# Kernel tuning notes

Hardware: AMD Instinct MI355X
Metric: run time of the kernel (lower is better)

## Reference

```python
import jax, jax.numpy as jnp
import numpy as np

N_REACHES = 4096
N_STEPS = 96
DT = 3600.0  # routing timestep (s), default from MuskingumCungeRouter


def safe_pow(base, exp, eps=1e-6):
    # AD-safe power: exp(e * log(max(b, eps)))
    return jnp.exp(exp * jnp.log(jnp.maximum(base, eps)))


def setup_inputs() -> dict:
    key = jax.random.key(0)
    ks = jax.random.split(key, 10)
    n, T = N_REACHES, N_STEPS
    u = lambda k, lo, hi, shape: jax.random.uniform(k, shape, minval=lo, maxval=hi)
    lateral_inflows = u(ks[0], 0.0, 5.0, (T, n))          # m^3/s lateral inflow
    initial_Q = u(ks[1], 0.1, 10.0, (n,))
    lengths = u(ks[2], 500.0, 10000.0, (n,))              # reach length (m)
    slopes = u(ks[3], 1e-4, 0.05, (n,))                   # bed slope
    manning_n = u(ks[4], 0.02, 0.08, (n,))
    width_coef = u(ks[5], 2.0, 10.0, (n,))
    width_exp = u(ks[6], 0.4, 0.6, (n,))                  # ~0.5 typical
    depth_coef = u(ks[7], 0.2, 0.6, (n,))
    depth_exp = u(ks[8], 0.25, 0.35, (n,))                # ~0.3 typical
    # Strictly lower-triangular sparse adjacency: reach i receives from j < i
    # (valid topological order), ~4 upstream links per reach on average.
    upstream_mask = jnp.tril(jax.random.uniform(ks[9], (n, n)) < (4.0 / n), k=-1)
    is_outlet = jnp.arange(n) == n - 1
    return dict(lateral_inflows=lateral_inflows, initial_Q=initial_Q,
                lengths=lengths, slopes=slopes, manning_n=manning_n,
                width_coef=width_coef, width_exp=width_exp,
                depth_coef=depth_coef, depth_exp=depth_exp,
                upstream_mask=upstream_mask, is_outlet=is_outlet)


def _mc_coeffs(Q, L, S, mn, wc, we, dc, de, dt):
    """Vectorized Muskingum-Cunge coefficients for all reaches.

    Faithful fusion of compute_channel_geometry -> compute_velocity_manning ->
    compute_celerity -> compute_muskingum_params. Q here is Q_ref = max(state.Q, 0.1),
    which only depends on the previous state, so hoisting out of the per-reach
    scan is mathematically identical to the original.
    """
    Qs = jnp.maximum(Q, 0.01)
    W = wc * safe_pow(Qs, we)
    D = dc * safe_pow(Qs, de)
    A = W * D
    R = A / (W + 2.0 * D)                      # hydraulic radius
    safe_S = jnp.maximum(S, 1e-6)
    V = (1.0 / jnp.maximum(mn, 1e-3)) * safe_pow(R, 2.0 / 3.0) * jnp.sqrt(safe_S)
    c = jnp.maximum((5.0 / 3.0) * V, 0.01)     # kinematic wave celerity
    K = jnp.maximum(L / c, dt * 0.1)
    X = jnp.clip(0.5 * (1.0 - Q / (W * c * safe_S * L + 1e-6)), 0.0, 0.5)
    den = 2.0 * K * (1.0 - X) + dt
    C0 = jnp.maximum((dt - 2.0 * K * X) / den, 0.0)
    C1 = jnp.maximum((dt + 2.0 * K * X) / den, 0.0)
    C2 = jnp.maximum((2.0 * K * (1.0 - X) - dt) / den, 0.0)
    tot = C0 + C1 + C2
    return C0 / tot, C1 / tot, C2 / tot


def _route(lateral_inflows, initial_Q, lengths, slopes, manning_n,
           width_coef, width_exp, depth_coef, depth_exp,
           upstream_mask, is_outlet, dt=DT):
    n = lengths.shape[0]

    def step(state, lateral):
        Q, Q_prev, I_prev = state
        Q_ref = jnp.maximum(Q, 0.1)
        C0, C1, C2 = _mc_coeffs(Q_ref, lengths, slopes, manning_n,
                                width_coef, width_exp, depth_coef, depth_exp, dt)

        # Sequential topological sweep: masked reduction over already-routed reaches.
        def process(Q_acc, i):
            upstream_Q = jnp.sum(jnp.where(upstream_mask[i], Q_acc, 0.0))
            I_curr = upstream_Q + lateral[i]
            Q_out = jnp.maximum(C0[i] * I_curr + C1[i] * I_prev[i] + C2[i] * Q_prev[i], 0.0)
            return Q_acc.at[i].set(Q_out), I_curr

        Q_final, I_all = jax.lax.scan(process, jnp.zeros(n, lateral.dtype), jnp.arange(n))
        outlet_Q = jnp.sum(jnp.where(is_outlet, Q_final, 0.0))
        return (Q_final, Q, I_all), outlet_Q

    init = (initial_Q, initial_Q, jnp.zeros(n, initial_Q.dtype))
    _, outlet_series = jax.lax.scan(step, init, lateral_inflows)
    return outlet_series  # [n_timesteps]


def reference(lateral_inflows, initial_Q, lengths, slopes, manning_n,
              width_coef, width_exp, depth_coef, depth_exp,
              upstream_mask, is_outlet):
    return _route(lateral_inflows, initial_Q, lengths, slopes, manning_n,
                  width_coef, width_exp, depth_coef, depth_exp,
                  upstream_mask, is_outlet)
```

## Files before the change

### kernel.cpp

```cpp
#include <hip/hip_runtime.h>

#define NR 4096
#define NT 96
#define NNZ_CAP 10240
#define SREM_CAP 4096
#define LONG_CAP 4096
#define WLDS 8
#define SSTR 4112
#define SHORTLAG 7
#define DHIST 32
#define DTSTEP 3600.0f
#define LOG2_1E6 -19.931568f

__device__ __forceinline__ float RCP(float x) { return __builtin_amdgcn_rcpf(x); }
__device__ __forceinline__ float EXP2(float x) { return __builtin_amdgcn_exp2f(x); }
__device__ __forceinline__ float LOG2(float x) { return __builtin_amdgcn_logf(x); }

__device__ __forceinline__ void phase_barrier() {
  asm volatile("s_waitcnt lgkmcnt(0) vmcnt(6)" ::: "memory");
  __builtin_amdgcn_s_barrier();
  asm volatile("" ::: "memory");
}

__global__ void mc_build(const int* __restrict__ mask, int* __restrict__ rowBase,
                         int* __restrict__ rowCnt, int* __restrict__ gctr,
                         unsigned short* __restrict__ cols) {
  __shared__ unsigned short tmp[80];
  __shared__ int baseS;
  int row = blockIdx.x;
  int lane = threadIdx.x;
  const int* rs = mask + (size_t)row * NR;
  int total = 0;
  for (int j0 = 0; j0 < NR; j0 += 64) {
    int j = j0 + lane;
    int pred = (rs[j] != 0);
    unsigned long long m = __ballot(pred);
    if (pred) {
      int pos = total + __popcll(m & ((1ull << lane) - 1ull));
      if (pos < 80) tmp[pos] = (unsigned short)j;
    }
    total += __popcll(m);
  }
  if (total > 80) total = 80;
  if (lane == 0) {
    int b = atomicAdd(gctr, total);
    rowBase[row] = b;
    rowCnt[row] = total;
    baseS = b;
  }
  __syncthreads();
  int base = baseS;
  for (int e = lane; e < total; e += 64) {
    int p = base + e;
    if (p < NNZ_CAP) cols[p] = tmp[e];
  }
}

__global__ __launch_bounds__(1024) void mc_prep(
    const int* __restrict__ rowBase, const int* __restrict__ rowCnt,
    const int* __restrict__ gctr, const unsigned short* __restrict__ colsOld,
    unsigned short* __restrict__ orderG, unsigned short* __restrict__ levNG,
    unsigned short* __restrict__ scolG, unsigned int* __restrict__ sremMeta,
    unsigned int* __restrict__ longMeta, unsigned short* __restrict__ sremG,
    unsigned short* __restrict__ longG, unsigned char* __restrict__ lsG,
    int* __restrict__ meta) {
  __shared__ unsigned short cols_s[NNZ_CAP];
  __shared__ unsigned char lev_s[NR];
  __shared__ unsigned short newid_s[NR];
  __shared__ unsigned short order_s[NR];
  __shared__ unsigned char lsrc_s[NR];
  __shared__ int cnt[1024];
  __shared__ int sbuf[1024];
  __shared__ int flagA[40];
  __shared__ int maxLevS;
  const int tid = threadIdx.x;
  int nnz = gctr[0];
  if (nnz > NNZ_CAP) nnz = NNZ_CAP;
  for (int e = tid; e < nnz; e += 1024) cols_s[e] = colsOld[e];
  for (int i = tid; i < 40; i += 1024) flagA[i] = 0;

  int b_r[4], e_r[4];
#pragma unroll
  for (int k = 0; k < 4; ++k) {
    int i = 4 * tid + k;
    int b = rowBase[i];
    if (b > NNZ_CAP) b = NNZ_CAP;
    int e = b + rowCnt[i];
    if (e > NNZ_CAP) e = NNZ_CAP;
    b_r[k] = b;
    e_r[k] = e;
    lev_s[i] = 0;
    lsrc_s[i] = 0;
  }
  if (tid == 0) maxLevS = 0;
  __syncthreads();

  for (int pass = 0; pass < 34; ++pass) {
    int ch = 0;
#pragma unroll
    for (int k = 0; k < 4; ++k) {
      int i = 4 * tid + k;
      int lv = 0;
      for (int e = b_r[k]; e < e_r[k]; ++e) {
        int l2 = (int)lev_s[cols_s[e]] + 1;
        lv = lv > l2 ? lv : l2;
      }
      if (lv > 60) lv = 60;
      if (lv > (int)lev_s[i]) {
        lev_s[i] = (unsigned char)lv;
        ch = 1;
      }
    }
    if (ch) flagA[pass] = 1;
    __syncthreads();
    if (flagA[pass] == 0) break;
  }
  int lm = 0;
#pragma unroll
  for (int k = 0; k < 4; ++k) {
    int l = lev_s[4 * tid + k];
    lm = lm > l ? lm : l;
  }
  atomicMax(&maxLevS, lm);
  __syncthreads();
  const int maxLev = maxLevS;
  if (tid == 0) {
    meta[0] = maxLev + 1;
    meta[2] = (maxLev >= 32) ? 1 : 0;
  }
  if (maxLev >= 32) {
#pragma unroll
    for (int k = 0; k < 4; ++k) {
      int i = 4 * tid + k;
      orderG[i] = (unsigned short)i;
      levNG[i] = (unsigned short)lev_s[i];
    }
    return;
  }

  cnt[tid] = 0;
  __syncthreads();
  int bkt_r[4];
#pragma unroll
  for (int k = 0; k < 4; ++k) {
    int i = 4 * tid + k;
    int d = e_r[k] - b_r[k];
    if (d > 31) d = 31;
    int bkt = ((int)lev_s[i]) * 32 + d;
    bkt_r[k] = bkt;
    atomicAdd(&cnt[bkt], 1);
  }
  __syncthreads();
  int v = cnt[tid];
  sbuf[tid] = v;
  __syncthreads();
  for (int off = 1; off < 1024; off <<= 1) {
    int add = tid >= off ? sbuf[tid - off] : 0;
    __syncthreads();
    sbuf[tid] += add;
    __syncthreads();
  }
  cnt[tid] = sbuf[tid] - v;
  __syncthreads();
#pragma unroll
  for (int k = 0; k < 4; ++k) {
    int i = 4 * tid + k;
    int pos = atomicAdd(&cnt[bkt_r[k]], 1);
    order_s[pos] = (unsigned short)i;
    newid_s[i] = (unsigned short)pos;
  }
  __syncthreads();

#pragma unroll
  for (int k = 0; k < 4; ++k) {
    int p = 4 * tid + k;
    int oldi = order_s[p];
    orderG[p] = (unsigned short)oldi;
    int lp = (int)lev_s[oldi];
    levNG[p] = (unsigned short)lp;
    int b = rowBase[oldi];
    if (b > NNZ_CAP) b = NNZ_CAP;
    int e = b + rowCnt[oldi];
    if (e > NNZ_CAP) e = NNZ_CAP;
    int nS = 0, nR = 0, nL = 0;
    for (int ee = b; ee < e; ++ee) {
      int lag = lp - (int)lev_s[cols_s[ee]];
      if (lag <= SHORTLAG) {
        if (nS < 4) ++nS; else ++nR;
      } else ++nL;
    }
    if (nR > 63) nR = 63;
    if (nL > 63) nL = 63;
    int sB = nR ? atomicAdd(&meta[4], nR) : 0;
    int lB = nL ? atomicAdd(&meta[5], nL) : 0;
    if (sB > SREM_CAP) sB = SREM_CAP;
    if (sB + nR > SREM_CAP) nR = SREM_CAP - sB;
    if (lB > LONG_CAP) lB = LONG_CAP;
    if (lB + nL > LONG_CAP) nL = LONG_CAP - lB;
    unsigned short sc[4] = {4096, 4096, 4096, 4096};
    int iS = 0, cR = 0, cL = 0;
    for (int ee = b; ee < e; ++ee) {
      int cOld = cols_s[ee];
      int cN = newid_s[cOld];
      int lag = lp - (int)lev_s[cOld];
      if (lag <= SHORTLAG) {
        if (iS < 4) sc[iS++] = (unsigned short)cN;
        else if (cR < nR) { sremG[sB + cR] = (unsigned short)cN; ++cR; }
      } else {
        if (cL < nL) { longG[lB + cL] = (unsigned short)cN; ++cL; }
        lsrc_s[cN] = 1;
      }
    }
    scolG[4 * p + 0] = sc[0];
    scolG[4 * p + 1] = sc[1];
    scolG[4 * p + 2] = sc[2];
    scolG[4 * p + 3] = sc[3];
    sremMeta[p] = (unsigned)sB | ((unsigned)nR << 20) | ((unsigned)iS << 26);
    longMeta[p] = (unsigned)lB | ((unsigned)nL << 20);
  }
  if (tid == 0) meta[1] = newid_s[NR - 1];
  __syncthreads();
#pragma unroll
  for (int k = 0; k < 4; ++k) {
    int p = 4 * tid + k;
    lsG[p] = lsrc_s[p];
  }
}

__global__ void mc_permlat(const float* __restrict__ lat,
                           const unsigned short* __restrict__ orderG,
                           float* __restrict__ latP) {
  int g = blockIdx.x * 256 + threadIdx.x;
  int t = g >> 12, p = g & 4095;
  latP[g] = lat[t * NR + orderG[p]];
}

__global__ __launch_bounds__(1024, 4) void mc_route(
    const float* __restrict__ lat, const float* __restrict__ latP,
    const float* __restrict__ initQ, const float* __restrict__ Lg,
    const float* __restrict__ Sg, const float* __restrict__ mng,
    const float* __restrict__ wcg, const float* __restrict__ weg,
    const float* __restrict__ dcg, const float* __restrict__ deg,
    const int* __restrict__ rowBase, const int* __restrict__ rowCnt,
    const unsigned short* __restrict__ colsOld,
    const unsigned short* __restrict__ orderG,
    const unsigned short* __restrict__ levNG,
    const unsigned short* __restrict__ scolG,
    const unsigned int* __restrict__ sremMeta,
    const unsigned int* __restrict__ longMeta,
    const unsigned short* __restrict__ sremG,
    const unsigned short* __restrict__ longG,
    const unsigned char* __restrict__ lsG, const int* __restrict__ meta,
    float* Qhist, float* __restrict__ out, int usePerm) {
  __shared__ float win_s[WLDS * SSTR];
  __shared__ unsigned short srem_s[SREM_CAP];
  __shared__ unsigned short long_s[LONG_CAP];
  const int tid = threadIdx.x;
  const int nlv = meta[0];
  const int fb = meta[2];
  const int outletNew = meta[1];
  const float* latB = usePerm ? latP : lat;

  if (!fb) {
    int sc_r[4][4];
    int lev_r[4], io_r[4], ls_r[4], wOff_r[4], nsc_r[4];
    unsigned int smeta_r[4], lmeta_r[4];
    const float* latcol_r[4];
    float lwc_r[4], we_r[4], ldc_r[4], de_r[4], lvk_r[4], lgSL_r[4], L_r[4];
    float ip_r[4], q1_r[4], q2_r[4], latN_r[4];
    float latv_r[4], sup_r[4], C0_r[4], C1_r[4], C2_r[4];

    int nSrem = meta[4];
    if (nSrem > SREM_CAP) nSrem = SREM_CAP;
    int nLong = meta[5];
    if (nLong > LONG_CAP) nLong = LONG_CAP;
    for (int e = tid; e < nSrem; e += 1024) srem_s[e] = sremG[e];
    for (int e = tid; e < nLong; e += 1024) long_s[e] = longG[e];
    if (tid < WLDS) win_s[tid * SSTR + 4096] = 0.f;

#pragma unroll
    for (int k = 0; k < 4; ++k) {
      int p = tid + k * 1024;
      int oldi = orderG[p];
      lev_r[k] = (int)levNG[p];
      uint2 cc = *(const uint2*)(scolG + 4 * p);
      sc_r[k][0] = cc.x & 0xFFFFu;
      sc_r[k][1] = cc.x >> 16;
      sc_r[k][2] = cc.y & 0xFFFFu;
      sc_r[k][3] = cc.y >> 16;
      smeta_r[k] = sremMeta[p];
      nsc_r[k] = (int)(smeta_r[k] >> 26);
      lmeta_r[k] = longMeta[p];
      ls_r[k] = (int)lsG[p];
      io_r[k] = (p == outletNew);
      float Lv = Lg[oldi];
      float sS = fmaxf(Sg[oldi], 1e-6f);
      float mnv = fmaxf(mng[oldi], 1e-3f);
      lvk_r[k] = 0.7369656f + 0.5f * LOG2(sS) - LOG2(mnv);
      lgSL_r[k] = LOG2(sS * Lv);
      L_r[k] = Lv;
      lwc_r[k] = LOG2(wcg[oldi]);
      we_r[k] = weg[oldi];
      ldc_r[k] = LOG2(dcg[oldi]);
      de_r[k] = deg[oldi];
      float q0 = initQ[oldi];
      q1_r[k] = q0;
      q2_r[k] = q0;
      ip_r[k] = 0.f;
      wOff_r[k] = 0;
      latcol_r[k] = latB + (usePerm ? p : oldi);
      latN_r[k] = *latcol_r[k];
    }
    __syncthreads();

#define BG(k, tt)                                                               \
  {                                                                             \
    latv_r[k] = latN_r[k];                                                      \
    int tn = (tt) + 1;                                                          \
    tn = tn < NT ? tn : NT - 1;                                                 \
    latN_r[k] = latcol_r[k][tn << 12];                                          \
    const int wB = wOff_r[k];                                                   \
    float v0 = win_s[wB + sc_r[k][0]];                                          \
    float v1 = win_s[wB + sc_r[k][1]];                                          \
    float v23 = 0.f;                                                            \
    if (nsc_r[k] > 2)                                                           \
      v23 = win_s[wB + sc_r[k][2]] + win_s[wB + sc_r[k][3]];                    \
    float ssum = 0.f;                                                           \
    const int sC = (int)((smeta_r[k] >> 20) & 63);                              \
    if (sC) {                                                                   \
      const int sB = (int)(smeta_r[k] & 0xFFFFFu);                              \
      for (int e = 0; e < sC; ++e) ssum += win_s[wB + srem_s[sB + e]];          \
    }                                                                           \
    float lsum = 0.f;                                                           \
    const int lC = (int)(lmeta_r[k] >> 20);                                     \
    if (lC) {                                                                   \
      const int lB = (int)(lmeta_r[k] & 0xFFFFFu);                              \
      const float* qb = Qhist + (((tt) & (DHIST - 1)) << 12);                   \
      for (int e = 0; e < lC; ++e) lsum += qb[long_s[lB + e]];                  \
    }                                                                           \
    sup_r[k] = ((v0 + v1) + v23) + (ssum + lsum);                               \
    float Qref = fmaxf(q1_r[k], 0.1f);                                          \
    float lq = LOG2(Qref);                                                      \
    float lgW = fmaf(we_r[k], lq, lwc_r[k]);                                    \
    float W = EXP2(lgW);                                                        \
    float aD = fmaf(de_r[k], lq, ldc_r[k]);                                     \
    float Dd = EXP2(aD);                                                        \
    float lgR = fmaxf(lgW + aD - LOG2(fmaf(2.f, Dd, W)), LOG2_1E6);             \
    float lgc = fmaf(0.66666667f, lgR, lvk_r[k]);                               \
    float K = fmaxf(L_r[k] * EXP2(-lgc), 360.f);                                \
    float ratio = EXP2(lq - lgW - lgc - lgSL_r[k]);                             \
    float X = fmaxf(fmaf(-0.5f, ratio, 0.5f), 0.f);                             \
    float twoK = K + K;                                                         \
    float twoKX = twoK * X;                                                     \
    C0_r[k] = fmaxf(DTSTEP - twoKX, 0.f);                                       \
    C1_r[k] = DTSTEP + twoKX;                                                   \
    C2_r[k] = fmaxf(twoK - twoKX - DTSTEP, 0.f);                                \
  }

#define BC(k, tt)                                                               \
  {                                                                             \
    const int p = tid + (k)*1024;                                               \
    float inv = RCP(C0_r[k] + C1_r[k] + C2_r[k]);                               \
    float Icurr = sup_r[k] + latv_r[k];                                         \
    float Qout = fmaxf(                                                         \
        (C0_r[k] * Icurr + C1_r[k] * ip_r[k] + C2_r[k] * q2_r[k]) * inv, 0.f);  \
    win_s[wOff_r[k] + p] = Qout;                                                \
    if (ls_r[k]) Qhist[(((tt) & (DHIST - 1)) << 12) | p] = Qout;                \
    if (io_r[k]) out[tt] = Qout;                                                \
    ip_r[k] = Icurr;                                                            \
    q2_r[k] = q1_r[k];                                                          \
    q1_r[k] = Qout;                                                             \
    wOff_r[k] = (wOff_r[k] == (WLDS - 1) * SSTR) ? 0 : wOff_r[k] + SSTR;        \
  }

    for (int s = 0; s < nlv - 1; ++s) {
#pragma unroll
      for (int k = 0; k < 4; ++k) {
        int t = s - lev_r[k];
        if ((unsigned)t < (unsigned)NT) {
          BG(k, t);
          BC(k, t);
        }
      }
      phase_barrier();
    }
    for (int s = nlv - 1; s < NT; ++s) {
      int t0 = s - lev_r[0], t1 = s - lev_r[1], t2 = s - lev_r[2],
          t3 = s - lev_r[3];
      BG(0, t0);
      BG(1, t1);
      BG(2, t2);
      BG(3, t3);
      BC(0, t0);
      BC(1, t1);
      BC(2, t2);
      BC(3, t3);
      phase_barrier();
    }
    for (int s = NT; s < NT + nlv - 1; ++s) {
#pragma unroll
      for (int k = 0; k < 4; ++k) {
        int t = s - lev_r[k];
        if ((unsigned)t < (unsigned)NT) {
          BG(k, t);
          BC(k, t);
        }
      }
      phase_barrier();
    }
  } else {
    unsigned short* colsF = (unsigned short*)win_s;
    int b_r[4], e_r[4], lev_r[4];
    float lwc_r[4], we_r[4], ldc_r[4], de_r[4], lvk_r[4], SL_r[4], L_r[4];
    float ip_r[4], q1_r[4], q2_r[4];
    for (int e = tid; e < NNZ_CAP; e += 1024) colsF[e] = colsOld[e];
#pragma unroll
    for (int k = 0; k < 4; ++k) {
      int i = tid + k * 1024;
      lev_r[k] = (int)levNG[i];
      int b = rowBase[i];
      if (b > NNZ_CAP) b = NNZ_CAP;
      int e = b + rowCnt[i];
      if (e > NNZ_CAP) e = NNZ_CAP;
      b_r[k] = b;
      e_r[k] = e;
      float Lv = Lg[i];
      float sS = fmaxf(Sg[i], 1e-6f);
      float mnv = fmaxf(mng[i], 1e-3f);
      lvk_r[k] = 0.7369656f + 0.5f * LOG2(sS) - LOG2(mnv);
      SL_r[k] = sS * Lv;
      L_r[k] = Lv;
      lwc_r[k] = LOG2(wcg[i]);
      we_r[k] = weg[i];
      ldc_r[k] = LOG2(dcg[i]);
      de_r[k] = deg[i];
      float q0 = initQ[i];
      q1_r[k] = q0;
      q2_r[k] = q0;
      ip_r[k] = 0.f;
    }
    __syncthreads();
    for (int t = 0; t < NT; ++t) {
      for (int l = 0; l < nlv; ++l) {
#pragma unroll
        for (int k = 0; k < 4; ++k) {
          if (lev_r[k] == l) {
            int i = tid + k * 1024;
            float latv = lat[t * NR + i];
            float Qref = fmaxf(q1_r[k], 0.1f);
            float lq = LOG2(Qref);
            float lgW = fmaf(we_r[k], lq, lwc_r[k]);
            float W = EXP2(lgW);
            float aD = fmaf(de_r[k], lq, ldc_r[k]);
            float Dd = EXP2(aD);
            float lgR = fmaxf(lgW + aD - LOG2(fmaf(2.f, Dd, W)), LOG2_1E6);
            float c = fmaxf(EXP2(fmaf(0.66666667f, lgR, lvk_r[k])), 0.01f);
            float K = fmaxf(L_r[k] * RCP(c), 360.f);
            float X =
                fmaxf(0.5f - 0.5f * Qref * RCP(fmaf(W * c, SL_r[k], 1e-6f)), 0.f);
            float twoKX = 2.f * K * X;
            float C0 = fmaxf(DTSTEP - twoKX, 0.f);
            float C1 = DTSTEP + twoKX;
            float C2 = fmaxf(2.f * K - twoKX - DTSTEP, 0.f);
            float inv = RCP(C0 + C1 + C2);
            float sup = 0.f;
            for (int e = b_r[k]; e < e_r[k]; ++e) sup += Qhist[colsF[e]];
            float Icurr = sup + latv;
            float Qout =
                fmaxf((C0 * Icurr + C1 * ip_r[k] + C2 * q2_r[k]) * inv, 0.f);
            Qhist[i] = Qout;
            ip_r[k] = Icurr;
            q2_r[k] = q1_r[k];
            q1_r[k] = Qout;
            if (i == NR - 1) out[t] = Qout;
          }
        }
        __syncthreads();
      }
    }
  }
}

extern "C" void kernel_launch(void* const* d_in, const int* in_sizes, int n_in,
                              void* d_out, int out_size, void* d_ws, size_t ws_size,
                              hipStream_t stream) {
  const float* lat = (const float*)d_in[0];
  const float* iQ = (const float*)d_in[1];
  const float* Lg = (const float*)d_in[2];
  const float* Sg = (const float*)d_in[3];
  const float* mng = (const float*)d_in[4];
  const float* wcg = (const float*)d_in[5];
  const float* weg = (const float*)d_in[6];
  const float* dcg = (const float*)d_in[7];
  const float* deg = (const float*)d_in[8];
  const int* mask = (const int*)d_in[9];
  float* out = (float*)d_out;

  char* w = (char*)d_ws;
  int* rowBase = (int*)w;                        w += NR * 4;
  int* rowCnt = (int*)w;                         w += NR * 4;
  int* gctr = (int*)w;                           w += 16;
  int* meta = (int*)w;                           w += 32;
  unsigned short* colsOld = (unsigned short*)w;  w += NNZ_CAP * 2;
  unsigned short* orderG = (unsigned short*)w;   w += NR * 2;
  unsigned short* levNG = (unsigned short*)w;    w += NR * 2;
  unsigned short* scolG = (unsigned short*)w;    w += NR * 4 * 2;
  unsigned int* sremMeta = (unsigned int*)w;     w += NR * 4;
  unsigned int* longMeta = (unsigned int*)w;     w += NR * 4;
  unsigned short* sremG = (unsigned short*)w;    w += SREM_CAP * 2;
  unsigned short* longG = (unsigned short*)w;    w += LONG_CAP * 2;
  unsigned char* lsG = (unsigned char*)w;        w += NR;
  w += 16 - ((size_t)w & 15);
  float* Qhist = (float*)w;                      w += (size_t)DHIST * NR * 4;
  float* latP = (float*)w;                       w += (size_t)NT * NR * 4;
  size_t need = (size_t)(w - (char*)d_ws);
  int usePerm = (ws_size >= need) ? 1 : 0;

  hipMemsetAsync(gctr, 0, 48, stream);
  mc_build<<<NR, 64, 0, stream>>>(mask, rowBase, rowCnt, gctr, colsOld);
  mc_prep<<<1, 1024, 0, stream>>>(rowBase, rowCnt, gctr, colsOld, orderG, levNG,
                                  scolG, sremMeta, longMeta, sremG, longG, lsG,
                                  meta);
  if (usePerm)
    mc_permlat<<<(NT * NR) / 256, 256, 0, stream>>>(lat, orderG, latP);
  mc_route<<<1, 1024, 0, stream>>>(lat, latP, iQ, Lg, Sg, mng, wcg, weg, dcg,
                                   deg, rowBase, rowCnt, colsOld, orderG, levNG,
                                   scolG, sremMeta, longMeta, sremG, longG, lsG,
                                   meta, Qhist, out, usePerm);
}
```

Baseline: 505.3 us.

## Use byte-offset column indices, merge gather/compute macros, wave-shuffle scan

Column indices are pre-shifted to byte offsets, so LDS gathers skip the index scaling, and the short-column loads become unconditional by padding with a zero slot. The separate gather and compute phases are merged into one BODY macro, which drops the per-reach staging registers for C0-C2, sup and latv. The setup kernel's Hillis-Steele block scan is replaced with a wave-shuffle scan, and the barrier now lets more vector loads stay outstanding. The main risk is that fusing the phases removes interleaving across the four reaches, which may expose LDS and global latency.

```diff
diff --git a/kernel.cpp b/kernel.cpp
--- a/kernel.cpp
+++ b/kernel.cpp
@@ -17,7 +17,7 @@
 __device__ __forceinline__ float LOG2(float x) { return __builtin_amdgcn_logf(x); }
 
 __device__ __forceinline__ void phase_barrier() {
-  asm volatile("s_waitcnt lgkmcnt(0) vmcnt(6)" ::: "memory");
+  asm volatile("s_waitcnt lgkmcnt(0) vmcnt(12)" ::: "memory");
   __builtin_amdgcn_s_barrier();
   asm volatile("" ::: "memory");
 }
@@ -70,7 +70,7 @@
   __shared__ unsigned short order_s[NR];
   __shared__ unsigned char lsrc_s[NR];
   __shared__ int cnt[1024];
-  __shared__ int sbuf[1024];
+  __shared__ int ws16[16];
   __shared__ int flagA[40];
   __shared__ int maxLevS;
   const int tid = threadIdx.x;
@@ -151,16 +151,30 @@
     atomicAdd(&cnt[bkt], 1);
   }
   __syncthreads();
-  int v = cnt[tid];
-  sbuf[tid] = v;
-  __syncthreads();
-  for (int off = 1; off < 1024; off <<= 1) {
-    int add = tid >= off ? sbuf[tid - off] : 0;
+  {
+    int v = cnt[tid];
+    int lane = tid & 63, wid = tid >> 6;
+    int x = v;
+#pragma unroll
+    for (int off = 1; off < 64; off <<= 1) {
+      int y = __shfl_up(x, off);
+      if (lane >= off) x += y;
+    }
+    if (lane == 63) ws16[wid] = x;
     __syncthreads();
-    sbuf[tid] += add;
+    if (wid == 0) {
+      int wv = (lane < 16) ? ws16[lane] : 0;
+#pragma unroll
+      for (int off = 1; off < 16; off <<= 1) {
+        int y = __shfl_up(wv, off);
+        if (lane >= off) wv += y;
+      }
+      if (lane < 16) ws16[lane] = wv;
+    }
     __syncthreads();
-  }
-  cnt[tid] = sbuf[tid] - v;
+    int base = wid ? ws16[wid - 1] : 0;
+    cnt[tid] = base + x - v;
+  }
   __syncthreads();
 #pragma unroll
   for (int k = 0; k < 4; ++k) {
@@ -197,17 +211,17 @@
     if (sB + nR > SREM_CAP) nR = SREM_CAP - sB;
     if (lB > LONG_CAP) lB = LONG_CAP;
     if (lB + nL > LONG_CAP) nL = LONG_CAP - lB;
-    unsigned short sc[4] = {4096, 4096, 4096, 4096};
+    unsigned short sc[4] = {16384, 16384, 16384, 16384};
     int iS = 0, cR = 0, cL = 0;
     for (int ee = b; ee < e; ++ee) {
       int cOld = cols_s[ee];
       int cN = newid_s[cOld];
       int lag = lp - (int)lev_s[cOld];
       if (lag <= SHORTLAG) {
-        if (iS < 4) sc[iS++] = (unsigned short)cN;
-        else if (cR < nR) { sremG[sB + cR] = (unsigned short)cN; ++cR; }
+        if (iS < 4) sc[iS++] = (unsigned short)(cN << 2);
+        else if (cR < nR) { sremG[sB + cR] = (unsigned short)(cN << 2); ++cR; }
       } else {
-        if (cL < nL) { longG[lB + cL] = (unsigned short)cN; ++cL; }
+        if (cL < nL) { longG[lB + cL] = (unsigned short)(cN << 2); ++cL; }
         lsrc_s[cN] = 1;
       }
     }
@@ -215,7 +229,7 @@
     scolG[4 * p + 1] = sc[1];
     scolG[4 * p + 2] = sc[2];
     scolG[4 * p + 3] = sc[3];
-    sremMeta[p] = (unsigned)sB | ((unsigned)nR << 20) | ((unsigned)iS << 26);
+    sremMeta[p] = (unsigned)sB | ((unsigned)nR << 20);
     longMeta[p] = (unsigned)lB | ((unsigned)nL << 20);
   }
   if (tid == 0) meta[1] = newid_s[NR - 1];
@@ -263,12 +277,11 @@
 
   if (!fb) {
     int sc_r[4][4];
-    int lev_r[4], io_r[4], ls_r[4], wOff_r[4], nsc_r[4];
+    int lev_r[4], io_r[4], ls_r[4], wOff_r[4];
     unsigned int smeta_r[4], lmeta_r[4];
     const float* latcol_r[4];
     float lwc_r[4], we_r[4], ldc_r[4], de_r[4], lvk_r[4], lgSL_r[4], L_r[4];
     float ip_r[4], q1_r[4], q2_r[4], latN_r[4];
-    float latv_r[4], sup_r[4], C0_r[4], C1_r[4], C2_r[4];
 
     int nSrem = meta[4];
     if (nSrem > SREM_CAP) nSrem = SREM_CAP;
@@ -289,7 +302,6 @@
       sc_r[k][2] = cc.y & 0xFFFFu;
       sc_r[k][3] = cc.y >> 16;
       smeta_r[k] = sremMeta[p];
-      nsc_r[k] = (int)(smeta_r[k] >> 26);
       lmeta_r[k] = longMeta[p];
       ls_r[k] = (int)lsG[p];
       io_r[k] = (p == outletNew);
@@ -313,32 +325,32 @@
     }
     __syncthreads();
 
-#define BG(k, tt)                                                               \
+#define BODY(k, tt)                                                             \
   {                                                                             \
-    latv_r[k] = latN_r[k];                                                      \
+    const int p = tid + (k)*1024;                                               \
+    const float latv = latN_r[k];                                               \
     int tn = (tt) + 1;                                                          \
     tn = tn < NT ? tn : NT - 1;                                                 \
     latN_r[k] = latcol_r[k][tn << 12];                                          \
-    const int wB = wOff_r[k];                                                   \
-    float v0 = win_s[wB + sc_r[k][0]];                                          \
-    float v1 = win_s[wB + sc_r[k][1]];                                          \
-    float v23 = 0.f;                                                            \
-    if (nsc_r[k] > 2)                                                           \
-      v23 = win_s[wB + sc_r[k][2]] + win_s[wB + sc_r[k][3]];                    \
+    const char* wb = (const char*)win_s + wOff_r[k];                            \
+    float v0 = *(const float*)(wb + sc_r[k][0]);                                \
+    float v1 = *(const float*)(wb + sc_r[k][1]);                                \
+    float v2 = *(const float*)(wb + sc_r[k][2]);                                \
+    float v3 = *(const float*)(wb + sc_r[k][3]);                                \
     float ssum = 0.f;                                                           \
     const int sC = (int)((smeta_r[k] >> 20) & 63);                              \
     if (sC) {                                                                   \
       const int sB = (int)(smeta_r[k] & 0xFFFFFu);                              \
-      for (int e = 0; e < sC; ++e) ssum += win_s[wB + srem_s[sB + e]];          \
+      for (int e = 0; e < sC; ++e)                                              \
+        ssum += *(const float*)(wb + srem_s[sB + e]);                           \
     }                                                                           \
     float lsum = 0.f;                                                           \
     const int lC = (int)(lmeta_r[k] >> 20);                                     \
     if (lC) {                                                                   \
       const int lB = (int)(lmeta_r[k] & 0xFFFFFu);                              \
-      const float* qb = Qhist + (((tt) & (DHIST - 1)) << 12);                   \
-      for (int e = 0; e < lC; ++e) lsum += qb[long_s[lB + e]];                  \
+      const char* qb = (const char*)Qhist + (((tt) & 31) << 14);                \
+      for (int e = 0; e < lC; ++e) lsum += *(const float*)(qb + long_s[lB + e]);\
     }                                                                           \
-    sup_r[k] = ((v0 + v1) + v23) + (ssum + lsum);                               \
     float Qref = fmaxf(q1_r[k], 0.1f);                                          \
     float lq = LOG2(Qref);                                                      \
     float lgW = fmaf(we_r[k], lq, lwc_r[k]);                                    \
@@ -352,59 +364,44 @@
     float X = fmaxf(fmaf(-0.5f, ratio, 0.5f), 0.f);                             \
     float twoK = K + K;                                                         \
     float twoKX = twoK * X;                                                     \
-    C0_r[k] = fmaxf(DTSTEP - twoKX, 0.f);                                       \
-    C1_r[k] = DTSTEP + twoKX;                                                   \
-    C2_r[k] = fmaxf(twoK - twoKX - DTSTEP, 0.f);                                \
-  }
-
-#define BC(k, tt)                                                               \
-  {                                                                             \
-    const int p = tid + (k)*1024;                                               \
-    float inv = RCP(C0_r[k] + C1_r[k] + C2_r[k]);                               \
-    float Icurr = sup_r[k] + latv_r[k];                                         \
-    float Qout = fmaxf(                                                         \
-        (C0_r[k] * Icurr + C1_r[k] * ip_r[k] + C2_r[k] * q2_r[k]) * inv, 0.f);  \
-    win_s[wOff_r[k] + p] = Qout;                                                \
-    if (ls_r[k]) Qhist[(((tt) & (DHIST - 1)) << 12) | p] = Qout;                \
+    float C0 = fmaxf(DTSTEP - twoKX, 0.f);                                      \
+    float C1 = DTSTEP + twoKX;                                                  \
+    float C2 = fmaxf(twoK - twoKX - DTSTEP, 0.f);                               \
+    float inv = RCP(C0 + C1 + C2);                                              \
+    float sup = ((v0 + v1) + (v2 + v3)) + (ssum + lsum);                        \
+    float Icurr = sup + latv;                                                   \
+    float Qout = fmaxf((C0 * Icurr + C1 * ip_r[k] + C2 * q2_r[k]) * inv, 0.f);  \
+    *(float*)((char*)win_s + wOff_r[k] + (p << 2)) = Qout;                      \
+    if (ls_r[k]) Qhist[(((tt) & 31) << 12) | p] = Qout;                         \
     if (io_r[k]) out[tt] = Qout;                                                \
     ip_r[k] = Icurr;                                                            \
     q2_r[k] = q1_r[k];                                                          \
     q1_r[k] = Qout;                                                             \
-    wOff_r[k] = (wOff_r[k] == (WLDS - 1) * SSTR) ? 0 : wOff_r[k] + SSTR;        \
+    wOff_r[k] =                                                                 \
+        (wOff_r[k] == (WLDS - 1) * SSTR * 4) ? 0 : wOff_r[k] + SSTR * 4;        \
   }
 
     for (int s = 0; s < nlv - 1; ++s) {
 #pragma unroll
       for (int k = 0; k < 4; ++k) {
         int t = s - lev_r[k];
-        if ((unsigned)t < (unsigned)NT) {
-          BG(k, t);
-          BC(k, t);
-        }
+        if ((unsigned)t < (unsigned)NT) BODY(k, t);
       }
       phase_barrier();
     }
     for (int s = nlv - 1; s < NT; ++s) {
-      int t0 = s - lev_r[0], t1 = s - lev_r[1], t2 = s - lev_r[2],
-          t3 = s - lev_r[3];
-      BG(0, t0);
-      BG(1, t1);
-      BG(2, t2);
-      BG(3, t3);
-      BC(0, t0);
-      BC(1, t1);
-      BC(2, t2);
-      BC(3, t3);
-      phase_barrier();
-    }
-    for (int s = NT; s < NT + nlv - 1; ++s) {
 #pragma unroll
       for (int k = 0; k < 4; ++k) {
         int t = s - lev_r[k];
-        if ((unsigned)t < (unsigned)NT) {
-          BG(k, t);
-          BC(k, t);
-        }
+        BODY(k, t);
+      }
+      phase_barrier();
+    }
+    for (int s = NT; s < NT + nlv - 1; ++s) {
+#pragma unroll
+      for (int k = 0; k < 4; ++k) {
+        int t = s - lev_r[k];
+        if ((unsigned)t < (unsigned)NT) BODY(k, t);
       }
       phase_barrier();
     }
```

Measured after the change: 478.9 us. -5.2%, faster.
